# Kernel optimization log

Hardware: AMD Instinct MI355X
Metric: run time of the kernel (lower is better)

The kernel has to match this reference:

```python
import jax, jax.numpy as jnp
import numpy as np

B = 8; C = 256; NH = 8; CH = C // NH; MLP_H = 4 * C; EPS = 1e-5
SIZES = [(56, 56), (28, 28), (14, 14), (7, 7)]  # scales 2..5; scale1 (112x112) passes through


def _layernorm(x, g, b):
    mu = jnp.mean(x, -1, keepdims=True)
    var = jnp.mean((x - mu) ** 2, -1, keepdims=True)
    return (x - mu) * jax.lax.rsqrt(var + EPS) * g + b


def _dwconv(x, w, b, pad):
    # x: [B, C, H, W], w: [C, 1, k, k] depthwise
    out = jax.lax.conv_general_dilated(
        x, w, (1, 1), [(pad, pad), (pad, pad)],
        feature_group_count=x.shape[1],
        dimension_numbers=('NCHW', 'OIHW', 'NCHW'))
    return out + b[None, :, None, None]


def _cpe(x, w, b, size):
    # ConvPosEnc: depthwise 3x3 conv residual on image tokens, cls untouched
    Hh, Ww = size
    Bb, N, Cc = x.shape
    cls_tok, img = x[:, :1], x[:, 1:]
    feat = img.transpose(0, 2, 1).reshape(Bb, Cc, Hh, Ww)
    feat = _dwconv(feat, w, b, 1) + feat
    img = feat.reshape(Bb, Cc, Hh * Ww).transpose(0, 2, 1)
    return jnp.concatenate([cls_tok, img], axis=1)


def _crpe(q, v, ws, bs, size):
    # ConvRelPosEnc: window->head split {3:2, 5:3, 7:3}; EV_hat = q * dwconv(v)
    Hh, Ww = size
    Bb, h, N, Ch = q.shape
    q_img, v_img = q[:, :, 1:], v[:, :, 1:]
    v_map = v_img.transpose(0, 1, 3, 2).reshape(Bb, h * Ch, Hh, Ww)
    splits = [2 * Ch, 3 * Ch, 3 * Ch]
    start = 0; outs = []
    for i, win in enumerate((3, 5, 7)):
        part = v_map[:, start:start + splits[i]]
        outs.append(_dwconv(part, ws[i], bs[i], win // 2))
        start += splits[i]
    conv_v = jnp.concatenate(outs, 1).reshape(Bb, h, Ch, Hh * Ww).transpose(0, 1, 3, 2)
    ev = q_img * conv_v  # [B, h, HW, Ch]
    return jnp.pad(ev, ((0, 0), (0, 0), (1, 0), (0, 0)))  # zero row for cls token


def _factor_att(x, qkv_w, proj_w, proj_b, crpe_ws, crpe_bs, size):
    Bb, N, Cc = x.shape
    qkv = (x @ qkv_w.T).reshape(Bb, N, 3, NH, CH).transpose(2, 0, 3, 1, 4)
    q, k, v = qkv[0], qkv[1], qkv[2]
    k_sm = jax.nn.softmax(k, axis=2)                       # softmax over tokens
    kv = jnp.einsum('bhnk,bhnv->bhkv', k_sm, v)            # [B,h,Ch,Ch]
    fa = jnp.einsum('bhnk,bhkv->bhnv', q, kv)              # [B,h,N,Ch]
    cr = _crpe(q, v, crpe_ws, crpe_bs, size)
    out = (CH ** -0.5 * fa + cr).transpose(0, 2, 1, 3).reshape(Bb, N, Cc)
    return out @ proj_w.T + proj_b


def _interp(x, out_size, size):
    # bilinear (align_corners=False) on image tokens; cls token passes through
    Bb, N, Cc = x.shape
    Hh, Ww = size
    cls_tok, img = x[:, :1], x[:, 1:]
    feat = img.transpose(0, 2, 1).reshape(Bb, Cc, Hh, Ww)
    feat = jax.image.resize(feat, (Bb, Cc, out_size[0], out_size[1]),
                            method='bilinear', antialias=False)
    img = feat.reshape(Bb, Cc, -1).transpose(0, 2, 1)
    return jnp.concatenate([cls_tok, img], axis=1)


def _mlp(x, w1, b1, w2, b2):
    h = jax.nn.gelu(x @ w1.T + b1, approximate=False)
    return h @ w2.T + b2


def _forward(x1, x2, x3, x4, x5, cpe_w, cpe_b, n1_g, n1_b, qkv_w, proj_w, proj_b,
             crpe_w3, crpe_b3, crpe_w5, crpe_b5, crpe_w7, crpe_b7,
             n2_g, n2_b, fc1_w, fc1_b, fc2_w, fc2_b):
    xs = [x2, x3, x4, x5]
    curs = []
    for i in range(4):  # fixed set of 4 scales (not a data-dim loop)
        xi = _cpe(xs[i], cpe_w[i], cpe_b[i], SIZES[i])
        cur = _layernorm(xi, n1_g[i], n1_b[i])
        cur = _factor_att(cur, qkv_w[i], proj_w[i], proj_b[i],
                          (crpe_w3[i], crpe_w5[i], crpe_w7[i]),
                          (crpe_b3[i], crpe_b5[i], crpe_b7[i]), SIZES[i])
        xs[i] = xi
        curs.append(cur)
    c2, c3, c4, c5 = curs
    s2, s3, s4, s5 = SIZES
    # only the interpolations actually used in the residual sums (source has dead ones)
    c2n = c2 + _interp(c3, s2, s3) + _interp(c4, s2, s4)
    c3n = c3 + _interp(c4, s3, s4) + _interp(c2, s3, s2)
    c4n = c4 + _interp(c5, s4, s5) + _interp(c2, s4, s2)
    c5n = c5 + _interp(c4, s5, s4) + _interp(c2, s5, s2)
    curs = [c2n, c3n, c4n, c5n]
    for i in range(4):
        xs[i] = xs[i] + curs[i]
        cur = _layernorm(xs[i], n2_g[i], n2_b[i])
        cur = _mlp(cur, fc1_w, fc1_b, fc2_w, fc2_b)  # MLP shared across scales
        xs[i] = xs[i] + cur
    return (x1, xs[0], xs[1], xs[2], xs[3])


def setup_inputs() -> dict:
    key = jax.random.key(0)
    ks = iter(jax.random.split(key, 40))
    def nrm(shape, scale=1.0):
        return jax.random.normal(next(ks), shape, jnp.float32) * scale
    W = 0.02
    inp = {}
    inp['x1'] = nrm((B, 1 + 112 * 112, C))
    for j, (h, w) in enumerate(SIZES):
        inp['x%d' % (j + 2)] = nrm((B, 1 + h * w, C))
    inp['cpe_w'] = nrm((4, C, 1, 3, 3), W); inp['cpe_b'] = jnp.zeros((4, C))
    inp['n1_g'] = jnp.ones((4, C)); inp['n1_b'] = jnp.zeros((4, C))
    inp['qkv_w'] = nrm((4, 3 * C, C), W)
    inp['proj_w'] = nrm((4, C, C), W); inp['proj_b'] = jnp.zeros((4, C))
    inp['crpe_w3'] = nrm((4, 2 * CH, 1, 3, 3), W); inp['crpe_b3'] = jnp.zeros((4, 2 * CH))
    inp['crpe_w5'] = nrm((4, 3 * CH, 1, 5, 5), W); inp['crpe_b5'] = jnp.zeros((4, 3 * CH))
    inp['crpe_w7'] = nrm((4, 3 * CH, 1, 7, 7), W); inp['crpe_b7'] = jnp.zeros((4, 3 * CH))
    inp['n2_g'] = jnp.ones((4, C)); inp['n2_b'] = jnp.zeros((4, C))
    inp['fc1_w'] = nrm((MLP_H, C), W); inp['fc1_b'] = jnp.zeros((MLP_H,))
    inp['fc2_w'] = nrm((C, MLP_H), W); inp['fc2_b'] = jnp.zeros((C,))
    return inp


def reference(x1, x2, x3, x4, x5, cpe_w, cpe_b, n1_g, n1_b, qkv_w, proj_w, proj_b,
              crpe_w3, crpe_b3, crpe_w5, crpe_b5, crpe_w7, crpe_b7,
              n2_g, n2_b, fc1_w, fc1_b, fc2_w, fc2_b):
    return _forward(x1, x2, x3, x4, x5, cpe_w, cpe_b, n1_g, n1_b, qkv_w, proj_w, proj_b,
                    crpe_w3, crpe_b3, crpe_w5, crpe_b5, crpe_w7, crpe_b7,
                    n2_g, n2_b, fc1_w, fc1_b, fc2_w, fc2_b)
```

## Files before the change

kernel.cpp:

```cpp
#include <hip/hip_runtime.h>
#include <math.h>

typedef unsigned short u16;
typedef __attribute__((ext_vector_type(8))) short bf16x8;
typedef __attribute__((ext_vector_type(4))) float f32x4;

#define MP 36864
#define OUTOFF0 25692160ull

#define DEV __device__ __forceinline__
#define AS1 __attribute__((address_space(1)))
#define AS3 __attribute__((address_space(3)))

DEV u16 f2bf(float x) {
  union { float f; unsigned u; } v; v.f = x;
  unsigned r = v.u + 0x7fffu + ((v.u >> 16) & 1u);
  return (u16)(r >> 16);
}
DEV float bf2f(u16 x) {
  union { unsigned u; float f; } v; v.u = ((unsigned)x) << 16;
  return v.f;
}

struct alignas(8) u16x4s { u16 x, y, z, w; };
struct alignas(16) U16x8 { u16 d[8]; };

DEV int rs_s(int row)   { return (row >= 25600) + (row >= 33792) + (row >= 35840); }
DEV int selPB(int s)    { return s == 0 ? 0 : s == 1 ? 25600 : s == 2 ? 33792 : 35840; }
DEV int selNPAD(int s)  { return s == 0 ? 3200 : s == 1 ? 1024 : s == 2 ? 256 : 128; }
DEV int selN(int s)     { return s == 0 ? 3137 : s == 1 ? 785 : s == 2 ? 197 : 50; }
DEV int selH(int s)     { return s == 0 ? 56 : s == 1 ? 28 : s == 2 ? 14 : 7; }
DEV int selRO(int s)    { return s == 0 ? 0 : s == 1 ? 25096 : s == 2 ? 31376 : 32952; }
DEV size_t selKPB(int s){ return s == 0 ? 0ull : s == 1 ? 6553600ull : s == 2 ? 8650752ull : 9175040ull; }
DEV size_t selVPB(int s){ return s == 0 ? 0ull : s == 1 ? 7340032ull : s == 2 ? 11010048ull : 12845056ull; }
DEV int selNC(int s)    { return s == 0 ? 32 : s == 1 ? 8 : s == 2 ? 2 : 1; }
DEV int selNCB(int s)   { return s == 0 ? 0 : s == 1 ? 2048 : s == 2 ? 2560 : 2688; }

DEV void sbn(int row, int s, int& b, int& n) {
  int l = row - selPB(s);
  if (s == 0)      { b = l / 3200; n = l - b * 3200; }
  else if (s == 1) { b = l >> 10; n = l & 1023; }
  else if (s == 2) { b = l >> 8;  n = l & 255; }
  else             { b = l >> 7;  n = l & 127; }
}

DEV int xcd_swizzle(int orig, int nblk) {
  int q = nblk >> 3, r = nblk & 7;
  int xcd = orig & 7, lin = orig >> 3;
  return (xcd < r ? xcd * (q + 1) : r * (q + 1) + (xcd - r) * q) + lin;
}

__global__ void cvt_all(const float* __restrict__ qkv_w, const float* __restrict__ proj_w,
                        const float* __restrict__ fc1_w, const float* __restrict__ fc2_w,
                        u16* __restrict__ WQ, u16* __restrict__ WP,
                        u16* __restrict__ W1, u16* __restrict__ W2) {
  int i = blockIdx.x * 256 + threadIdx.x;
  if (i < 786432) WQ[i] = f2bf(qkv_w[i]);
  else if (i < 1048576) WP[i - 786432] = f2bf(proj_w[i - 786432]);
  else if (i < 1310720) W1[i - 1048576] = f2bf(fc1_w[i - 1048576]);
  else if (i < 1572864) W2[i - 1310720] = f2bf(fc2_w[i - 1310720]);
}

__global__ void tpw_cpe(const float* __restrict__ src, float* __restrict__ dst) {
  int i = blockIdx.y;
  int e = blockIdx.x * 256 + threadIdx.x;
  if (e < 2304) {
    int c = e / 9, k = e % 9;
    dst[i * 2304 + k * 256 + c] = src[i * 2304 + c * 9 + k];
  }
}

__global__ void copy_f4(const float4* __restrict__ src, float4* __restrict__ dst, int n4) {
  for (int i = blockIdx.x * blockDim.x + threadIdx.x; i < n4; i += gridDim.x * blockDim.x)
    dst[i] = src[i];
}

__global__ void cpe_ln_all(const float* __restrict__ x2, const float* __restrict__ x3,
                           const float* __restrict__ x4, const float* __restrict__ x5,
                           const float* __restrict__ WT, const float* __restrict__ cpe_b,
                           const float* __restrict__ n1g, const float* __restrict__ n1b,
                           float* __restrict__ XI, u16* __restrict__ T1) {
  int wid = threadIdx.x >> 6, lane = threadIdx.x & 63;
  int row = blockIdx.x * 4 + wid;
  if (row >= MP) return;
  int s = rs_s(row);
  int b, n; sbn(row, s, b, n);
  int N = selN(s), H = selH(s);
  int c4 = lane * 4;
  float4 v = make_float4(0.f, 0.f, 0.f, 0.f);
  if (n < N) {
    const float* x = s == 0 ? x2 : s == 1 ? x3 : s == 2 ? x4 : x5;
    v = *(const float4*)(x + ((size_t)b * N + n) * 256 + c4);
    if (n > 0) {
      int p = n - 1, h0 = p / H, w0 = p % H;
      float4 acc = *(const float4*)(cpe_b + s * 256 + c4);
      const float* wT = WT + s * 2304;
      #pragma unroll
      for (int kh = 0; kh < 3; ++kh) {
        int hh = h0 + kh - 1;
        if (hh < 0 || hh >= H) continue;
        #pragma unroll
        for (int kw = 0; kw < 3; ++kw) {
          int ww = w0 + kw - 1;
          if (ww < 0 || ww >= H) continue;
          float4 t = *(const float4*)(x + ((size_t)b * N + 1 + hh * H + ww) * 256 + c4);
          float4 wv = *(const float4*)(wT + (kh * 3 + kw) * 256 + c4);
          acc.x += t.x * wv.x; acc.y += t.y * wv.y;
          acc.z += t.z * wv.z; acc.w += t.w * wv.w;
        }
      }
      v.x += acc.x; v.y += acc.y; v.z += acc.z; v.w += acc.w;
    }
  }
  *(float4*)(XI + (size_t)row * 256 + c4) = v;
  float sm = v.x + v.y + v.z + v.w;
  #pragma unroll
  for (int off = 32; off; off >>= 1) sm += __shfl_down(sm, off);
  sm = __shfl(sm, 0);
  float mu = sm * (1.0f / 256.0f);
  float dx = v.x - mu, dy = v.y - mu, dz = v.z - mu, dw = v.w - mu;
  float q = dx * dx + dy * dy + dz * dz + dw * dw;
  #pragma unroll
  for (int off = 32; off; off >>= 1) q += __shfl_down(q, off);
  q = __shfl(q, 0);
  float rs = rsqrtf(q * (1.0f / 256.0f) + 1e-5f);
  float4 gg = *(const float4*)(n1g + s * 256 + c4);
  float4 bb = *(const float4*)(n1b + s * 256 + c4);
  u16x4s o;
  o.x = f2bf(dx * rs * gg.x + bb.x);
  o.y = f2bf(dy * rs * gg.y + bb.y);
  o.z = f2bf(dz * rs * gg.z + bb.z);
  o.w = f2bf(dw * rs * gg.w + bb.w);
  *(u16x4s*)(T1 + (size_t)row * 256 + c4) = o;
}

DEV void stage32(const u16* __restrict__ A, const u16* __restrict__ W,
                 u16* dst, int bm, int bn, int K, int k0) {
  int t = threadIdx.x, wv = t >> 6;
  u16* aD = dst;
  u16* bD = dst + 4096;
  #pragma unroll
  for (int iss = 0; iss < 2; ++iss) {
    int sI = iss * 256 + t;
    int row = sI >> 2, g = sI & 3;
    int gel = ((g ^ (row & 3)) << 3);
    __builtin_amdgcn_global_load_lds(
        (const AS1 void*)(A + (size_t)(bm + row) * K + k0 + gel),
        (AS3 void*)(aD + (size_t)(iss * 256 + wv * 64) * 8), 16, 0, 0);
    __builtin_amdgcn_global_load_lds(
        (const AS1 void*)(W + (size_t)(bn + row) * K + k0 + gel),
        (AS3 void*)(bD + (size_t)(iss * 256 + wv * 64) * 8), 16, 0, 0);
  }
}

DEV void mainloop(const u16* __restrict__ A, const u16* __restrict__ W, int K,
                  int bm, int bn, u16* lds, f32x4 (&acc)[4][4]) {
  int t = threadIdx.x, lane = t & 63, wv = t >> 6;
  int wr = wv >> 1, wc = wv & 1;
  const int nt = K >> 5;
  stage32(A, W, lds, bm, bn, K, 0);
  stage32(A, W, lds + 8192, bm, bn, K, 32);
  int buf = 0;
  for (int tt = 0; tt < nt; ++tt) {
    if (tt + 1 < nt) asm volatile("s_waitcnt vmcnt(4)" ::: "memory");
    else             asm volatile("s_waitcnt vmcnt(0)" ::: "memory");
    __builtin_amdgcn_s_barrier();
    asm volatile("" ::: "memory");
    if (tt + 2 < nt) {
      int nb = buf + 2; if (nb >= 3) nb -= 3;
      stage32(A, W, lds + nb * 8192, bm, bn, K, (tt + 2) << 5);
    }
    const u16* aS = lds + buf * 8192;
    const u16* bS = aS + 4096;
    bf16x8 af[4], bfr[4];
    #pragma unroll
    for (int m = 0; m < 4; ++m) {
      int row = wr * 64 + m * 16 + (lane & 15);
      int sg = (lane >> 4) ^ (row & 3);
      af[m] = *(const bf16x8*)(aS + row * 32 + sg * 8);
    }
    #pragma unroll
    for (int n = 0; n < 4; ++n) {
      int row = wc * 64 + n * 16 + (lane & 15);
      int sg = (lane >> 4) ^ (row & 3);
      bfr[n] = *(const bf16x8*)(bS + row * 32 + sg * 8);
    }
    #pragma unroll
    for (int m = 0; m < 4; ++m)
      #pragma unroll
      for (int n = 0; n < 4; ++n)
        acc[m][n] = __builtin_amdgcn_mfma_f32_16x16x32_bf16(af[m], bfr[n], acc[m][n], 0, 0, 0);
    buf += 1; if (buf >= 3) buf -= 3;
  }
}

DEV void epi_dump(const f32x4 (&acc)[4][4], int pass, float* eps) {
  int t = threadIdx.x, lane = t & 63, wv = t >> 6;
  int wr = wv >> 1, wc = wv & 1;
  if (wr != (pass >> 1)) return;
  #pragma unroll
  for (int mh = 0; mh < 2; ++mh) {
    int m = (pass & 1) * 2 + mh;
    #pragma unroll
    for (int n = 0; n < 4; ++n) {
      int col = wc * 64 + n * 16 + (lane & 15);
      #pragma unroll
      for (int rg = 0; rg < 4; ++rg)
        eps[(mh * 16 + ((lane >> 4) << 2) + rg) * 132 + col] = acc[m][n][rg];
    }
  }
}

template <bool GELU, bool BF16>
DEV void epi_rowmajor(const float* eps, int pass, void* outp, const float* bias,
                      int bm, int bn, int Nout) {
  int t = threadIdx.x;
  int lr = t >> 3, cb = (t & 7) * 4;
  int gr = bm + pass * 32 + lr;
  #pragma unroll
  for (int j = 0; j < 4; ++j) {
    int col = cb + j * 32;
    float4 f = *(const float4*)(eps + lr * 132 + col);
    int gc = bn + col;
    if (bias) {
      float4 bv = *(const float4*)(bias + gc);
      f.x += bv.x; f.y += bv.y; f.z += bv.z; f.w += bv.w;
    }
    if (GELU) {
      f.x /= (1.0f + __expf(-1.702f * f.x));
      f.y /= (1.0f + __expf(-1.702f * f.y));
      f.z /= (1.0f + __expf(-1.702f * f.z));
      f.w /= (1.0f + __expf(-1.702f * f.w));
    }
    if (BF16) {
      u16x4s p;
      p.x = f2bf(f.x); p.y = f2bf(f.y); p.z = f2bf(f.z); p.w = f2bf(f.w);
      *(u16x4s*)((u16*)outp + (size_t)gr * Nout + gc) = p;
    } else {
      *(float4*)((float*)outp + (size_t)gr * Nout + gc) = f;
    }
  }
}

template <bool GELU, bool BF16>
__launch_bounds__(256, 3)
__global__ void gemm_std(const u16* __restrict__ A, const u16* __restrict__ W,
                         const float* __restrict__ bias, void* __restrict__ outp,
                         int K, int Nout, int nnt) {
  __shared__ __align__(16) u16 lds[24576];
  int wg = xcd_swizzle(blockIdx.x, gridDim.x);
  int bm = (wg / nnt) << 7, bn = (wg % nnt) << 7;
  f32x4 acc[4][4] = {};
  mainloop(A, W, K, bm, bn, lds, acc);
  float* eps = (float*)lds;
  #pragma unroll
  for (int pass = 0; pass < 4; ++pass) {
    __syncthreads();
    epi_dump(acc, pass, eps);
    __syncthreads();
    epi_rowmajor<GELU, BF16>(eps, pass, outp, bias, bm, bn, Nout);
  }
}

__launch_bounds__(256, 3)
__global__ void qkv_gemm(const u16* __restrict__ A, const u16* __restrict__ WQ,
                         u16* __restrict__ Q16, u16* __restrict__ KP,
                         u16* __restrict__ VP) {
  __shared__ __align__(16) u16 lds[24576];
  int wg = xcd_swizzle(blockIdx.x, gridDim.x);
  int mt = wg / 6, ct = wg % 6;
  int bm = mt << 7, bn = ct << 7;
  int s = rs_s(bm);
  f32x4 acc[4][4] = {};
  mainloop(A, WQ + (size_t)s * 196608, 256, bm, bn, lds, acc);
  float* eps = (float*)lds;
  int b, nb; sbn(bm, s, b, nb);
  int NPAD = selNPAD(s);
  #pragma unroll
  for (int pass = 0; pass < 4; ++pass) {
    __syncthreads();
    epi_dump(acc, pass, eps);
    __syncthreads();
    if (ct < 2) {
      epi_rowmajor<false, true>(eps, pass, Q16, nullptr, bm, bn, 256);
    } else {
      int t = threadIdx.x;
      int c = t >> 1, half = t & 1;
      bool isK = (ct < 4);
      int cg = bn - (isK ? 256 : 512) + c;
      int n0 = nb + pass * 32 + half * 16;
      float vals[16];
      #pragma unroll
      for (int r = 0; r < 16; ++r) vals[r] = eps[(half * 16 + r) * 132 + c];
      U16x8 p0, p1;
      #pragma unroll
      for (int e = 0; e < 8; ++e) { p0.d[e] = f2bf(vals[e]); p1.d[e] = f2bf(vals[8 + e]); }
      u16* pbase = (isK ? KP : VP) + selKPB(s) + (size_t)(b * 256 + cg) * NPAD + n0;
      *(U16x8*)pbase = p0;
      *(U16x8*)(pbase + 8) = p1;
    }
  }
}

__launch_bounds__(256, 3)
__global__ void proj_gemm(const u16* __restrict__ A, const u16* __restrict__ WP,
                          const float* __restrict__ proj_b, float* __restrict__ CC) {
  __shared__ __align__(16) u16 lds[24576];
  int wg = xcd_swizzle(blockIdx.x, gridDim.x);
  int bm = (wg >> 1) << 7, bn = (wg & 1) << 7;
  int s = rs_s(bm);
  f32x4 acc[4][4] = {};
  mainloop(A, WP + (size_t)s * 65536, 256, bm, bn, lds, acc);
  float* eps = (float*)lds;
  #pragma unroll
  for (int pass = 0; pass < 4; ++pass) {
    __syncthreads();
    epi_dump(acc, pass, eps);
    __syncthreads();
    epi_rowmajor<false, false>(eps, pass, CC, proj_b + s * 256, bm, bn, 256);
  }
}

__launch_bounds__(256, 3)
__global__ void fc2_gemm(const u16* __restrict__ A, const u16* __restrict__ W2,
                         const float* __restrict__ fc2_b, const float* __restrict__ XI,
                         float* __restrict__ out) {
  __shared__ __align__(16) u16 lds[24576];
  int wg = xcd_swizzle(blockIdx.x, gridDim.x);
  int bm = (wg >> 1) << 7, bn = (wg & 1) << 7;
  f32x4 acc[4][4] = {};
  mainloop(A, W2, 1024, bm, bn, lds, acc);
  float* eps = (float*)lds;
  int s = rs_s(bm);
  int b, nb; sbn(bm, s, b, nb);
  int N = selN(s), RO = selRO(s);
  #pragma unroll
  for (int pass = 0; pass < 4; ++pass) {
    __syncthreads();
    epi_dump(acc, pass, eps);
    __syncthreads();
    int t = threadIdx.x;
    int lr = t >> 3, cb = (t & 7) * 4;
    int n = nb + pass * 32 + lr;
    if (n >= N) continue;
    int prow = bm + pass * 32 + lr;
    size_t orow = (size_t)RO + (size_t)b * N + n;
    #pragma unroll
    for (int j = 0; j < 4; ++j) {
      int col = cb + j * 32;
      float4 f = *(const float4*)(eps + lr * 132 + col);
      int gc = bn + col;
      float4 bv = *(const float4*)(fc2_b + gc);
      float4 rv = *(const float4*)(XI + (size_t)prow * 256 + gc);
      f.x += bv.x + rv.x; f.y += bv.y + rv.y;
      f.z += bv.z + rv.z; f.w += bv.w + rv.w;
      *(float4*)(out + OUTOFF0 + orow * 256 + gc) = f;
    }
  }
}

__global__ void vimg_fill(const u16* __restrict__ VP, u16* __restrict__ VPI) {
  int plane = blockIdx.x;
  int s = plane >> 11;
  int pc = plane & 2047;
  int H = selH(s), NPAD = selNPAD(s);
  const u16* vp = VP + selKPB(s) + (size_t)pc * NPAD;
  u16* vi = VPI + selVPB(s) + (size_t)pc * (H * 64);
  int tot = H * 64;
  for (int e = threadIdx.x; e < tot; e += 256) {
    int h = e >> 6, w = e & 63;
    vi[e] = (w < H) ? vp[1 + h * H + w] : (u16)0;
  }
}

__global__ void ksm_all(const u16* __restrict__ KP, float* __restrict__ mx,
                        float* __restrict__ se) {
  int s = blockIdx.z, b = blockIdx.y;
  int N = selN(s), NPAD = selNPAD(s);
  int wv = threadIdx.x >> 6, lane = threadIdx.x & 63;
  int cg = blockIdx.x * 4 + wv;
  const u16* kp = KP + selKPB(s) + (size_t)(b * 256 + cg) * NPAD;
  float m = -1e30f, sm = 0.f;
  for (int n = lane; n < N; n += 64) {
    float v = bf2f(kp[n]);
    float nm = fmaxf(m, v);
    sm = sm * __expf(m - nm) + __expf(v - nm);
    m = nm;
  }
  #pragma unroll
  for (int off = 1; off < 64; off <<= 1) {
    float mo = __shfl_xor(m, off), so = __shfl_xor(sm, off);
    float nm = fmaxf(m, mo);
    sm = sm * __expf(m - nm) + so * __expf(mo - nm);
    m = nm;
  }
  if (lane == 0) { mx[s * 2048 + b * 256 + cg] = m; se[s * 2048 + b * 256 + cg] = sm; }
}

__launch_bounds__(1024)
__global__ void kv_partial_all(const u16* __restrict__ KP, const u16* __restrict__ VP,
                               const float* __restrict__ mx, float* __restrict__ part) {
  __shared__ float kl[32][65];
  __shared__ float vl[32][65];
  int blk = blockIdx.x;
  int s = (blk >= selNCB(1)) + (blk >= selNCB(2)) + (blk >= selNCB(3));
  int local = blk - selNCB(s);
  int NC = selNC(s);
  int chunk = local % NC;
  int bh = local / NC;
  int b = bh >> 3, h = bh & 7;
  int N = selN(s), NPAD = selNPAD(s);
  int chunkrows = (N + NC - 1) / NC;
  const u16* kpb = KP + selKPB(s);
  const u16* vpb = VP + selKPB(s);
  int t = threadIdx.x;
  int i = t >> 5, j = t & 31;
  float acc = 0.f;
  int n0s = chunk * chunkrows, n1s = min(N, n0s + chunkrows);
  for (int n0 = n0s; n0 < n1s; n0 += 64) {
    #pragma unroll
    for (int e = t; e < 2048; e += 1024) {
      int c = e >> 6, nn = e & 63;
      int n = n0 + nn;
      bool ok = (n < n1s);
      kl[c][nn] = ok ? bf2f(kpb[(size_t)(b * 256 + h * 32 + c) * NPAD + n]) : -1e30f;
      vl[c][nn] = ok ? bf2f(vpb[(size_t)(b * 256 + h * 32 + c) * NPAD + n]) : 0.f;
    }
    __syncthreads();
    #pragma unroll
    for (int e = t; e < 2048; e += 1024) {
      int c = e >> 6, nn = e & 63;
      kl[c][nn] = __expf(kl[c][nn] - mx[s * 2048 + b * 256 + h * 32 + c]);
    }
    __syncthreads();
    #pragma unroll
    for (int nn = 0; nn < 64; ++nn) acc += kl[i][nn] * vl[j][nn];
    __syncthreads();
  }
  part[(size_t)blk * 1024 + t] = acc;
}

__global__ void kv_reduce_all(const float* __restrict__ part, const float* __restrict__ se,
                              float* __restrict__ kv) {
  int bh = blockIdx.x, s = blockIdx.y;
  int NC = selNC(s), base = selNCB(s);
  int t = threadIdx.x;
  int i = t >> 5;
  int b = bh >> 3, h = bh & 7;
  float sm = 0.f;
  for (int c = 0; c < NC; ++c) sm += part[(size_t)(base + bh * NC + c) * 1024 + t];
  kv[(size_t)s * 65536 + bh * 1024 + t] = sm / se[s * 2048 + b * 256 + h * 32 + i];
}

template <int KS, int C0>
__global__ void crpe_all(const u16* __restrict__ VPI, const float* __restrict__ w,
                         const float* __restrict__ bias, u16* __restrict__ CVPI, int CS) {
  constexpr int pad = KS / 2;
  int z = blockIdx.z;
  int s = (z >= 2) + (z >= 3) + (z >= 4);
  int sub = z - (s == 0 ? 0 : s + 1);
  int RS = (s == 0) ? 2 : 1;
  int H = selH(s);
  int c = blockIdx.x, b = blockIdx.y;
  int G = (H + 7) >> 3;
  int hpb = (H + RS - 1) / RS;
  int h0b = sub * hpb;
  int h1b = min(H, h0b + hpb);
  size_t plane = selVPB(s) + (size_t)(b * 256 + C0 + c) * (size_t)(H * 64);
  const u16* vp = VPI + plane;
  u16* op = CVPI + plane;
  float wreg[KS * KS];
  #pragma unroll
  for (int e = 0; e < KS * KS; ++e) wreg[e] = w[(s * CS + c) * KS * KS + e];
  float bb = bias[s * CS + c];
  int ntask = (h1b - h0b) * G;
  for (int task = threadIdx.x; task < ntask; task += 256) {
    int g = task % G;
    int h = h0b + task / G;
    int w0 = g << 3;
    float o[8];
    #pragma unroll
    for (int e = 0; e < 8; ++e) o[e] = bb;
    #pragma unroll
    for (int kh = 0; kh < KS; ++kh) {
      int hh = h + kh - pad;
      if (hh < 0 || hh >= H) continue;
      const u16* rowp = vp + hh * 64;
      U16x8 ch0 = {}, ch1, ch2;
      if (w0 >= 8) ch0 = *(const U16x8*)(rowp + w0 - 8);
      ch1 = *(const U16x8*)(rowp + w0);
      ch2 = *(const U16x8*)(rowp + w0 + 8);
      float tv[24];
      #pragma unroll
      for (int j2 = 8 - pad; j2 <= 15 + pad; ++j2) {
        u16 raw = (j2 < 8) ? ch0.d[j2] : (j2 < 16 ? ch1.d[j2 - 8] : ch2.d[j2 - 16]);
        tv[j2] = bf2f(raw);
      }
      #pragma unroll
      for (int kw = 0; kw < KS; ++kw) {
        float wv = wreg[kh * KS + kw];
        #pragma unroll
        for (int e = 0; e < 8; ++e) o[e] += tv[8 + e + kw - pad] * wv;
      }
    }
    U16x8 pk;
    #pragma unroll
    for (int e = 0; e < 8; ++e) pk.d[e] = f2bf(o[e]);
    *(U16x8*)(op + h * 64 + w0) = pk;
  }
}

__global__ void att_all(const u16* __restrict__ Q16, const u16* __restrict__ CVPI,
                        const float* __restrict__ kvg, u16* __restrict__ attp) {
  int s = blockIdx.z, b = blockIdx.y;
  int N = selN(s), H = selH(s);
  int n0 = blockIdx.x * 16;
  if (n0 >= N) return;
  __shared__ float kvl[8192];
  __shared__ float ql[256];
  __shared__ float cl[16][260];
  int t = threadIdx.x;
  int hw64 = H * 64;
  size_t rowbase = (size_t)selPB(s) + (size_t)b * selNPAD(s);
  const u16* cvb = CVPI + selVPB(s);
  for (int e = t; e < 8192; e += 256) kvl[e] = kvg[(size_t)s * 65536 + b * 8192 + e];
  for (int e = t; e < 4096; e += 256) {
    int c = e >> 4, nn = e & 15;
    int n = n0 + nn;
    float v = 0.f;
    if (n >= 1 && n < N) {
      int p = n - 1;
      v = bf2f(cvb[(size_t)(b * 256 + c) * hw64 + (p / H) * 64 + (p % H)]);
    }
    cl[nn][c] = v;
  }
  int h = t >> 5, j = t & 31;
  for (int nn = 0; nn < 16; ++nn) {
    int n = n0 + nn;
    if (n >= N) break;
    __syncthreads();
    ql[t] = bf2f(Q16[(rowbase + n) * 256 + t]);
    __syncthreads();
    float fa = 0.f;
    const float* kvh = kvl + h * 1024;
    #pragma unroll
    for (int k = 0; k < 32; ++k) fa += ql[h * 32 + k] * kvh[k * 32 + j];
    float v = 0.17677669529663687f * fa + ql[t] * cl[nn][t];
    attp[(rowbase + n) * 256 + t] = f2bf(v);
  }
}

DEV float4 bs4(const float* __restrict__ base, int Hs, int oh, int ow, int Hi, int c4) {
  float scale = (float)Hs / (float)Hi;
  float sy = (oh + 0.5f) * scale - 0.5f;
  float sx = (ow + 0.5f) * scale - 0.5f;
  float fy0 = floorf(sy), fx0 = floorf(sx);
  float fy = sy - fy0, fx = sx - fx0;
  int y0 = (int)fy0, x0 = (int)fx0;
  int y0c = min(max(y0, 0), Hs - 1), y1c = min(max(y0 + 1, 0), Hs - 1);
  int x0c = min(max(x0, 0), Hs - 1), x1c = min(max(x0 + 1, 0), Hs - 1);
  const float* ib = base + 256 + c4;
  float4 v00 = *(const float4*)(ib + (size_t)(y0c * Hs + x0c) * 256);
  float4 v01 = *(const float4*)(ib + (size_t)(y0c * Hs + x1c) * 256);
  float4 v10 = *(const float4*)(ib + (size_t)(y1c * Hs + x0c) * 256);
  float4 v11 = *(const float4*)(ib + (size_t)(y1c * Hs + x1c) * 256);
  float w00 = (1.f - fy) * (1.f - fx), w01 = (1.f - fy) * fx;
  float w10 = fy * (1.f - fx), w11 = fy * fx;
  float4 r;
  r.x = w00 * v00.x + w01 * v01.x + w10 * v10.x + w11 * v11.x;
  r.y = w00 * v00.y + w01 * v01.y + w10 * v10.y + w11 * v11.y;
  r.z = w00 * v00.z + w01 * v01.z + w10 * v10.z + w11 * v11.z;
  r.w = w00 * v00.w + w01 * v01.w + w10 * v10.w + w11 * v11.w;
  return r;
}

__global__ void combine_ln_all(float* __restrict__ XI, const float* __restrict__ CC,
                               const float* __restrict__ n2g, const float* __restrict__ n2b,
                               u16* __restrict__ T1) {
  int wid = threadIdx.x >> 6, lane = threadIdx.x & 63;
  int row = blockIdx.x * 4 + wid;
  if (row >= MP) return;
  int s = rs_s(row);
  int b, n; sbn(row, s, b, n);
  int N = selN(s), Hi = selH(s);
  int c4 = lane * 4;
  float4 v;
  if (n < N) {
    float4 add = *(const float4*)(CC + (size_t)row * 256 + c4);
    int sa = s == 0 ? 1 : s == 1 ? 2 : s == 2 ? 3 : 2;
    int sb_ = s == 0 ? 2 : 0;
    const float* baseA = CC + ((size_t)selPB(sa) + (size_t)b * selNPAD(sa)) * 256;
    const float* baseB = CC + ((size_t)selPB(sb_) + (size_t)b * selNPAD(sb_)) * 256;
    if (n == 0) {
      float4 a = *(const float4*)(baseA + c4);
      float4 bb2 = *(const float4*)(baseB + c4);
      add.x += a.x + bb2.x; add.y += a.y + bb2.y;
      add.z += a.z + bb2.z; add.w += a.w + bb2.w;
    } else {
      int p = n - 1, oh = p / Hi, ow = p % Hi;
      float4 a = bs4(baseA, selH(sa), oh, ow, Hi, c4);
      float4 bb2 = bs4(baseB, selH(sb_), oh, ow, Hi, c4);
      add.x += a.x + bb2.x; add.y += a.y + bb2.y;
      add.z += a.z + bb2.z; add.w += a.w + bb2.w;
    }
    float* xp = XI + (size_t)row * 256 + c4;
    v = *(const float4*)xp;
    v.x += add.x; v.y += add.y; v.z += add.z; v.w += add.w;
    *(float4*)xp = v;
  } else {
    v = make_float4(0.f, 0.f, 0.f, 0.f);
  }
  float sm = v.x + v.y + v.z + v.w;
  #pragma unroll
  for (int off = 32; off; off >>= 1) sm += __shfl_down(sm, off);
  sm = __shfl(sm, 0);
  float mu = sm * (1.0f / 256.0f);
  float dx = v.x - mu, dy = v.y - mu, dz = v.z - mu, dw = v.w - mu;
  float q = dx * dx + dy * dy + dz * dz + dw * dw;
  #pragma unroll
  for (int off = 32; off; off >>= 1) q += __shfl_down(q, off);
  q = __shfl(q, 0);
  float rs = rsqrtf(q * (1.0f / 256.0f) + 1e-5f);
  float4 gg = *(const float4*)(n2g + s * 256 + c4);
  float4 bb = *(const float4*)(n2b + s * 256 + c4);
  u16x4s o;
  o.x = f2bf(dx * rs * gg.x + bb.x);
  o.y = f2bf(dy * rs * gg.y + bb.y);
  o.z = f2bf(dz * rs * gg.z + bb.z);
  o.w = f2bf(dw * rs * gg.w + bb.w);
  *(u16x4s*)(T1 + (size_t)row * 256 + c4) = o;
}

extern "C" void kernel_launch(void* const* d_in, const int* in_sizes, int n_in,
                              void* d_out, int out_size, void* d_ws, size_t ws_size,
                              hipStream_t stream) {
  const float* x1 = (const float*)d_in[0];
  const float* x2 = (const float*)d_in[1];
  const float* x3 = (const float*)d_in[2];
  const float* x4 = (const float*)d_in[3];
  const float* x5 = (const float*)d_in[4];
  const float* cpe_w  = (const float*)d_in[5];
  const float* cpe_b  = (const float*)d_in[6];
  const float* n1_g   = (const float*)d_in[7];
  const float* n1_b   = (const float*)d_in[8];
  const float* qkv_w  = (const float*)d_in[9];
  const float* proj_w = (const float*)d_in[10];
  const float* proj_b = (const float*)d_in[11];
  const float* crpe_w3 = (const float*)d_in[12];
  const float* crpe_b3 = (const float*)d_in[13];
  const float* crpe_w5 = (const float*)d_in[14];
  const float* crpe_b5 = (const float*)d_in[15];
  const float* crpe_w7 = (const float*)d_in[16];
  const float* crpe_b7 = (const float*)d_in[17];
  const float* n2_g   = (const float*)d_in[18];
  const float* n2_b   = (const float*)d_in[19];
  const float* fc1_w  = (const float*)d_in[20];
  const float* fc1_b  = (const float*)d_in[21];
  const float* fc2_w  = (const float*)d_in[22];
  const float* fc2_b  = (const float*)d_in[23];

  float* ws = (float*)d_ws;
  float* XI   = ws;
  float* CC   = XI + 9437184;
  u16*   T1   = (u16*)(CC + 9437184);
  float* REG  = (float*)(T1 + 9437184);
  u16*   Q16  = (u16*)REG;
  u16*   KP   = Q16 + 9437184;
  u16*   VP   = KP + 9437184;
  u16*   VPI  = VP + 9437184;
  u16*   CVPI = VPI + 13762560;
  float* PRT  = (float*)CVPI;
  u16*   T2   = (u16*)REG;
  float* MX   = (float*)(CVPI + 13762560);
  float* SE   = MX + 8192;
  float* KV   = SE + 8192;
  u16*   WQ   = (u16*)(KV + 262144);
  u16*   WP   = WQ + 786432;
  u16*   W1   = WP + 262144;
  u16*   W2   = W1 + 262144;
  float* WT   = (float*)(W2 + 262144);

  float* out = (float*)d_out;

  cvt_all<<<6144, 256, 0, stream>>>(qkv_w, proj_w, fc1_w, fc2_w, WQ, WP, W1, W2);
  tpw_cpe<<<dim3(9, 4), 256, 0, stream>>>(cpe_w, WT);

  copy_f4<<<8192, 256, 0, stream>>>((const float4*)x1, (float4*)out, 25692160 / 4);

  cpe_ln_all<<<MP / 4, 256, 0, stream>>>(x2, x3, x4, x5, WT, cpe_b, n1_g, n1_b, XI, T1);

  qkv_gemm<<<288 * 6, 256, 0, stream>>>(T1, WQ, Q16, KP, VP);
  vimg_fill<<<8192, 256, 0, stream>>>(VP, VPI);

  ksm_all<<<dim3(64, 8, 4), 256, 0, stream>>>(KP, MX, SE);
  kv_partial_all<<<2752, 1024, 0, stream>>>(KP, VP, MX, PRT);
  kv_reduce_all<<<dim3(64, 4), 1024, 0, stream>>>(PRT, SE, KV);
  crpe_all<3, 0><<<dim3(64, 8, 5), 256, 0, stream>>>(VPI, crpe_w3, crpe_b3, CVPI, 64);
  crpe_all<5, 64><<<dim3(96, 8, 5), 256, 0, stream>>>(VPI, crpe_w5, crpe_b5, CVPI, 96);
  crpe_all<7, 160><<<dim3(96, 8, 5), 256, 0, stream>>>(VPI, crpe_w7, crpe_b7, CVPI, 96);
  att_all<<<dim3(197, 8, 4), 256, 0, stream>>>(Q16, CVPI, KV, T1);

  proj_gemm<<<288 * 2, 256, 0, stream>>>(T1, WP, proj_b, CC);

  combine_ln_all<<<MP / 4, 256, 0, stream>>>(XI, CC, n2_g, n2_b, T1);

  gemm_std<true, true><<<288 * 8, 256, 0, stream>>>(T1, W1, fc1_b, (void*)T2, 256, 1024, 8);
  fc2_gemm<<<288 * 2, 256, 0, stream>>>(T2, W2, fc2_b, XI, out);
}
```

Measured before the change: 446.5 us.

## Restructure att_all: bf16 kv, 32-row tiles, kv in registers, batched q staging

The kv matrix is now stored in bf16 instead of fp32, and each attention block handles 32 tokens instead of 16. All q rows are staged into shared memory up front, which removes the two per-row __syncthreads. Each thread keeps its kv column in registers and reads q with vectorized loads. This cuts per-block kv loading and synchronisation overhead, at the cost of bf16 rounding of kv and more registers per thread.

Measured after the change: 433.0 us. 1.03x faster.

```diff
diff --git a/kernel.cpp b/kernel.cpp
--- a/kernel.cpp
+++ b/kernel.cpp
@@ -441,7 +441,7 @@
 }
 
 __global__ void kv_reduce_all(const float* __restrict__ part, const float* __restrict__ se,
-                              float* __restrict__ kv) {
+                              u16* __restrict__ kvh) {
   int bh = blockIdx.x, s = blockIdx.y;
   int NC = selNC(s), base = selNCB(s);
   int t = threadIdx.x;
@@ -449,7 +449,7 @@
   int b = bh >> 3, h = bh & 7;
   float sm = 0.f;
   for (int c = 0; c < NC; ++c) sm += part[(size_t)(base + bh * NC + c) * 1024 + t];
-  kv[(size_t)s * 65536 + bh * 1024 + t] = sm / se[s * 2048 + b * 256 + h * 32 + i];
+  kvh[(size_t)s * 65536 + bh * 1024 + t] = f2bf(sm / se[s * 2048 + b * 256 + h * 32 + i]);
 }
 
 template <int KS, int C0>
@@ -510,42 +510,52 @@
   }
 }
 
+__launch_bounds__(256, 3)
 __global__ void att_all(const u16* __restrict__ Q16, const u16* __restrict__ CVPI,
-                        const float* __restrict__ kvg, u16* __restrict__ attp) {
+                        const u16* __restrict__ kvh, u16* __restrict__ attp) {
   int s = blockIdx.z, b = blockIdx.y;
   int N = selN(s), H = selH(s);
-  int n0 = blockIdx.x * 16;
+  int n0 = blockIdx.x * 32;
   if (n0 >= N) return;
-  __shared__ float kvl[8192];
-  __shared__ float ql[256];
-  __shared__ float cl[16][260];
+  __shared__ u16 kvl[8192];
+  __shared__ u16 ql[32][256];
+  __shared__ u16 cl[32][256];
   int t = threadIdx.x;
   int hw64 = H * 64;
   size_t rowbase = (size_t)selPB(s) + (size_t)b * selNPAD(s);
   const u16* cvb = CVPI + selVPB(s);
-  for (int e = t; e < 8192; e += 256) kvl[e] = kvg[(size_t)s * 65536 + b * 8192 + e];
-  for (int e = t; e < 4096; e += 256) {
-    int c = e >> 4, nn = e & 15;
+  const u16* kvsrc = kvh + (size_t)s * 65536 + (size_t)b * 8192;
+  for (int e = t; e < 1024; e += 256)
+    *(U16x8*)(kvl + e * 8) = *(const U16x8*)(kvsrc + e * 8);
+  for (int e = t; e < 1024; e += 256)
+    *(U16x8*)(&ql[0][0] + e * 8) = *(const U16x8*)(Q16 + (rowbase + n0) * 256 + e * 8);
+  for (int e = t; e < 8192; e += 256) {
+    int c = e >> 5, nn = e & 31;
     int n = n0 + nn;
-    float v = 0.f;
+    u16 v = 0;
     if (n >= 1 && n < N) {
       int p = n - 1;
-      v = bf2f(cvb[(size_t)(b * 256 + c) * hw64 + (p / H) * 64 + (p % H)]);
+      v = cvb[(size_t)(b * 256 + c) * hw64 + (p / H) * 64 + (p % H)];
     }
     cl[nn][c] = v;
   }
+  __syncthreads();
   int h = t >> 5, j = t & 31;
-  for (int nn = 0; nn < 16; ++nn) {
+  float kvr[32];
+  #pragma unroll
+  for (int k = 0; k < 32; ++k) kvr[k] = bf2f(kvl[(h * 32 + k) * 32 + j]);
+  for (int nn = 0; nn < 32; ++nn) {
     int n = n0 + nn;
     if (n >= N) break;
-    __syncthreads();
-    ql[t] = bf2f(Q16[(rowbase + n) * 256 + t]);
-    __syncthreads();
     float fa = 0.f;
-    const float* kvh = kvl + h * 1024;
-    #pragma unroll
-    for (int k = 0; k < 32; ++k) fa += ql[h * 32 + k] * kvh[k * 32 + j];
-    float v = 0.17677669529663687f * fa + ql[t] * cl[nn][t];
+    const U16x8* qp = (const U16x8*)(&ql[nn][h * 32]);
+    #pragma unroll
+    for (int seg = 0; seg < 4; ++seg) {
+      U16x8 qq = qp[seg];
+      #pragma unroll
+      for (int e = 0; e < 8; ++e) fa += bf2f(qq.d[e]) * kvr[seg * 8 + e];
+    }
+    float v = 0.17677669529663687f * fa + bf2f(ql[nn][t]) * bf2f(cl[nn][t]);
     attp[(rowbase + n) * 256 + t] = f2bf(v);
   }
 }
@@ -673,8 +683,8 @@
   u16*   T2   = (u16*)REG;
   float* MX   = (float*)(CVPI + 13762560);
   float* SE   = MX + 8192;
-  float* KV   = SE + 8192;
-  u16*   WQ   = (u16*)(KV + 262144);
+  u16*   KVH  = (u16*)(SE + 8192);
+  u16*   WQ   = KVH + 262144;
   u16*   WP   = WQ + 786432;
   u16*   W1   = WP + 262144;
   u16*   W2   = W1 + 262144;
@@ -694,11 +704,11 @@
 
   ksm_all<<<dim3(64, 8, 4), 256, 0, stream>>>(KP, MX, SE);
   kv_partial_all<<<2752, 1024, 0, stream>>>(KP, VP, MX, PRT);
-  kv_reduce_all<<<dim3(64, 4), 1024, 0, stream>>>(PRT, SE, KV);
+  kv_reduce_all<<<dim3(64, 4), 1024, 0, stream>>>(PRT, SE, KVH);
   crpe_all<3, 0><<<dim3(64, 8, 5), 256, 0, stream>>>(VPI, crpe_w3, crpe_b3, CVPI, 64);
   crpe_all<5, 64><<<dim3(96, 8, 5), 256, 0, stream>>>(VPI, crpe_w5, crpe_b5, CVPI, 96);
   crpe_all<7, 160><<<dim3(96, 8, 5), 256, 0, stream>>>(VPI, crpe_w7, crpe_b7, CVPI, 96);
-  att_all<<<dim3(197, 8, 4), 256, 0, stream>>>(Q16, CVPI, KV, T1);
+  att_all<<<dim3(99, 8, 4), 256, 0, stream>>>(Q16, CVPI, KVH, T1);
 
   proj_gemm<<<288 * 2, 256, 0, stream>>>(T1, WP, proj_b, CC);
 
```
